# Kernel tuning notes

Hardware: AMD Instinct MI355X
Metric: run time of the kernel (lower is better)

## Reference

```python
import jax, jax.numpy as jnp
import numpy as np

DIM = 512; HEADS = 8; DH = 64; LAND = 256; PINV_ITERS = 6; RES_K = 33
NCLS = 4; FEAT = 1024; NPATCH = 16384

def layernorm(x, g, b, eps=1e-5):
    mu = x.mean(-1, keepdims=True)
    var = ((x - mu) ** 2).mean(-1, keepdims=True)
    return (x - mu) * jax.lax.rsqrt(var + eps) * g + b

def moore_penrose_pinv(x, iters):
    abs_x = jnp.abs(x)
    z = jnp.swapaxes(x, -1, -2) / (jnp.max(abs_x.sum(-1)) * jnp.max(abs_x.sum(-2)))
    I = jnp.eye(x.shape[-1], dtype=x.dtype)
    for _ in range(iters):
        xz = x @ z
        z = 0.25 * z @ (13 * I - xz @ (15 * I - xz @ (7 * I - xz)))
    return z

def nystrom_attention(x, qkv_w, out_w, out_b, res_w):
    b, n, _ = x.shape
    pad = (-n) % LAND  # left-pad to multiple of num_landmarks
    xp = jnp.pad(x, ((0, 0), (pad, 0), (0, 0)))
    N = n + pad
    q, k, v = jnp.split(xp @ qkv_w, 3, axis=-1)
    to_h = lambda t: t.reshape(b, N, HEADS, DH).transpose(0, 2, 1, 3)  # b h N d
    q = to_h(q) * (DH ** -0.5); k = to_h(k); v = to_h(v)
    l = N // LAND
    ql = q.reshape(b, HEADS, LAND, l, DH).mean(3)  # landmark means
    kl = k.reshape(b, HEADS, LAND, l, DH).mean(3)
    a1 = jax.nn.softmax(jnp.einsum('bhnd,bhmd->bhnm', q, kl), -1)
    a2 = jax.nn.softmax(jnp.einsum('bhld,bhmd->bhlm', ql, kl), -1)
    a3 = jax.nn.softmax(jnp.einsum('bhld,bhnd->bhln', ql, k), -1)
    out = (a1 @ moore_penrose_pinv(a2, PINV_ITERS)) @ (a3 @ v)  # b h N d
    res = jax.lax.conv_general_dilated(v, res_w, (1, 1), ((RES_K // 2, RES_K // 2), (0, 0)),
        dimension_numbers=('NCHW', 'OIHW', 'NCHW'), feature_group_count=HEADS)
    out = (out + res).transpose(0, 2, 1, 3).reshape(b, N, HEADS * DH)
    return (out @ out_w + out_b)[:, -n:]

def ppeg(x, w7, b7, w5, b5, w3, b3, Hh, Ww):
    B, _, C = x.shape
    cls, feat = x[:, :1], x[:, 1:]
    img = feat.transpose(0, 2, 1).reshape(B, C, Hh, Ww)
    def dw(w, bias, ksz):
        p = ksz // 2
        y = jax.lax.conv_general_dilated(img, w, (1, 1), ((p, p), (p, p)),
            dimension_numbers=('NCHW', 'OIHW', 'NCHW'), feature_group_count=C)
        return y + bias[None, :, None, None]
    y = img + dw(w7, b7, 7) + dw(w5, b5, 5) + dw(w3, b3, 3)
    return jnp.concatenate([cls, y.reshape(B, C, Hh * Ww).transpose(0, 2, 1)], 1)

def setup_inputs():
    ks = jax.random.split(jax.random.key(0), 16)
    p = lambda i, shape, s=0.02: jax.random.normal(ks[i], shape, jnp.float32) * s
    z = lambda shape: jnp.zeros(shape, jnp.float32)
    o = lambda shape: jnp.ones(shape, jnp.float32)
    return {
        'data_x': jax.random.normal(ks[0], (NPATCH, FEAT), jnp.float32),
        'fc1_w': p(1, (FEAT, DIM)), 'fc1_b': z((DIM,)),
        'cls_token': jax.random.normal(ks[2], (1, 1, DIM), jnp.float32),
        'l1_norm_g': o((DIM,)), 'l1_norm_b': z((DIM,)),
        'l1_qkv_w': p(3, (DIM, 3 * HEADS * DH)), 'l1_out_w': p(4, (HEADS * DH, DIM)), 'l1_out_b': z((DIM,)),
        'l1_res_w': p(5, (HEADS, 1, RES_K, 1)),
        'ppeg_w7': p(6, (DIM, 1, 7, 7)), 'ppeg_b7': z((DIM,)),
        'ppeg_w5': p(7, (DIM, 1, 5, 5)), 'ppeg_b5': z((DIM,)),
        'ppeg_w3': p(8, (DIM, 1, 3, 3)), 'ppeg_b3': z((DIM,)),
        'l2_norm_g': o((DIM,)), 'l2_norm_b': z((DIM,)),
        'l2_qkv_w': p(9, (DIM, 3 * HEADS * DH)), 'l2_out_w': p(10, (HEADS * DH, DIM)), 'l2_out_b': z((DIM,)),
        'l2_res_w': p(11, (HEADS, 1, RES_K, 1)),
        'norm_g': o((DIM,)), 'norm_b': z((DIM,)),
        'fc2_w': p(12, (DIM, NCLS)), 'fc2_b': z((NCLS,)),
    }

def reference(data_x, fc1_w, fc1_b, cls_token, l1_norm_g, l1_norm_b, l1_qkv_w, l1_out_w, l1_out_b, l1_res_w, ppeg_w7, ppeg_b7, ppeg_w5, ppeg_b5, ppeg_w3, ppeg_b3, l2_norm_g, l2_norm_b, l2_qkv_w, l2_out_w, l2_out_b, l2_res_w, norm_g, norm_b, fc2_w, fc2_b):
    h = jax.nn.relu(data_x[None] @ fc1_w + fc1_b)  # [1, N, 512]
    H = h.shape[1]
    _H = int(np.ceil(np.sqrt(H)))
    add = _H * _H - H
    h = jnp.concatenate([h, h[:, :add]], 1)  # square-pad by wrap
    cls = jnp.broadcast_to(cls_token, (h.shape[0], 1, DIM))
    h = jnp.concatenate([cls, h], 1)
    h = h + nystrom_attention(layernorm(h, l1_norm_g, l1_norm_b), l1_qkv_w, l1_out_w, l1_out_b, l1_res_w)
    h = ppeg(h, ppeg_w7, ppeg_b7, ppeg_w5, ppeg_b5, ppeg_w3, ppeg_b3, _H, _H)
    h = h + nystrom_attention(layernorm(h, l2_norm_g, l2_norm_b), l2_qkv_w, l2_out_w, l2_out_b, l2_res_w)
    h = layernorm(h, norm_g, norm_b)[:, 0]
    return h @ fc2_w + fc2_b
```

## Files before the change

### kernel.cpp

```cpp
#include <hip/hip_runtime.h>
#include <hip/hip_bf16.h>

#define NPAD 16640
#define TOK  16385
#define CDIM 512
#define NHEAD 8
#define DHEAD 64
#define NLAND 256
#define LFAC  65
#define PAD0  255
#define NCHUNK 65
#define CGRP 2
#define NCG 33

typedef __attribute__((ext_vector_type(8))) short sh8;
typedef __attribute__((ext_vector_type(4))) float f4;

__device__ __forceinline__ float wave_sum(float v){
  #pragma unroll
  for(int o=32;o;o>>=1) v += __shfl_xor(v,o);
  return v;
}
__device__ __forceinline__ float wave_max(float v){
  #pragma unroll
  for(int o=32;o;o>>=1) v = fmaxf(v, __shfl_xor(v,o));
  return v;
}

__device__ __forceinline__ unsigned bfbits(float x){
  unsigned u = __float_as_uint(x);
  return (u + 0x7fffu + ((u >> 16) & 1u)) >> 16;
}
__device__ __forceinline__ float bf2f(short s){
  return __uint_as_float(((unsigned)(unsigned short)s) << 16);
}
__device__ __forceinline__ sh8 pack8f(float4 a, float4 b){
  sh8 r;
  r[0]=(short)bfbits(a.x); r[1]=(short)bfbits(a.y); r[2]=(short)bfbits(a.z); r[3]=(short)bfbits(a.w);
  r[4]=(short)bfbits(b.x); r[5]=(short)bfbits(b.y); r[6]=(short)bfbits(b.z); r[7]=(short)bfbits(b.w);
  return r;
}
#define MFMA16(a,b,c) __builtin_amdgcn_mfma_f32_16x16x32_bf16(a,b,c,0,0,0)

__device__ __forceinline__ void gload16(const void* g, void* l){
  __builtin_amdgcn_global_load_lds(
      (const __attribute__((address_space(1))) void*)g,
      (__attribute__((address_space(3))) void*)l, 16, 0, 0);
}

#define BAR_LGKM() do{ \
  asm volatile("s_waitcnt lgkmcnt(0)" ::: "memory"); \
  __builtin_amdgcn_s_barrier(); \
  __builtin_amdgcn_sched_barrier(0); \
}while(0)

__global__ void k_copyrow(float* dst, const float* __restrict__ src){
  dst[threadIdx.x] = src[threadIdx.x];
}

__global__ __launch_bounds__(256) void k_f2b(const float* __restrict__ in,
    short* __restrict__ out, int n8){
  int i = blockIdx.x*256 + threadIdx.x;
  if(i < n8){
    float4 a = *(const float4*)(in + (size_t)i*8);
    float4 b = *(const float4*)(in + (size_t)i*8 + 4);
    *(sh8*)(out + (size_t)i*8) = pack8f(a, b);
  }
}

__global__ __launch_bounds__(256) void k_ln_pad(const float* __restrict__ A,
    const float* __restrict__ g, const float* __restrict__ b, short* __restrict__ B){
  int w = threadIdx.x >> 6, lane = threadIdx.x & 63;
  int row = blockIdx.x*4 + w;
  short* out = B + (size_t)row*CDIM;
  int c = lane*8;
  if(row < PAD0){
    sh8 z = {0,0,0,0,0,0,0,0};
    *(sh8*)(out + c) = z;
    return;
  }
  const float* x = A + (size_t)(row-PAD0)*CDIM;
  float4 v0 = *(const float4*)(x + c);
  float4 v1 = *(const float4*)(x + c + 4);
  float xs[8] = {v0.x,v0.y,v0.z,v0.w,v1.x,v1.y,v1.z,v1.w};
  float s = 0;
  #pragma unroll
  for(int i=0;i<8;i++) s += xs[i];
  s = wave_sum(s);
  float mu = s * (1.f/512.f);
  float vs = 0;
  #pragma unroll
  for(int i=0;i<8;i++){ float d = xs[i]-mu; vs += d*d; }
  vs = wave_sum(vs) * (1.f/512.f);
  float rs = rsqrtf(vs + 1e-5f);
  float4 g0 = *(const float4*)(g + c); float4 g1 = *(const float4*)(g + c + 4);
  float4 b0 = *(const float4*)(b + c); float4 b1 = *(const float4*)(b + c + 4);
  float gg[8] = {g0.x,g0.y,g0.z,g0.w,g1.x,g1.y,g1.z,g1.w};
  float bb[8] = {b0.x,b0.y,b0.z,b0.w,b1.x,b1.y,b1.z,b1.w};
  sh8 o;
  #pragma unroll
  for(int i=0;i<8;i++) o[i] = (short)bfbits((xs[i]-mu)*rs*gg[i] + bb[i]);
  *(sh8*)(out + c) = o;
}

template<int MODE>
__global__ __launch_bounds__(512) void k_gemm_g(const short* __restrict__ A, int lda,
    const short* __restrict__ WT, int K, const float* __restrict__ bias,
    void* out0v, void* out1v, void* out2v, int M){
  __shared__ short As[2][256*32];
  __shared__ short Bs[2][128*32];
  int t = threadIdx.x, lane = t & 63, wv = t >> 6, g = lane >> 4, l15 = lane & 15;
  int nwg = gridDim.x * gridDim.y;
  int orig = blockIdx.y * gridDim.x + blockIdx.x;
  int qc = nwg >> 3, rc = nwg & 7, xcd = orig & 7, loc = orig >> 3;
  int wgid = (xcd < rc ? xcd*(qc+1) : rc*(qc+1) + (xcd - rc)*qc) + loc;
  int row0 = (wgid / gridDim.x) * 256, n0 = (wgid % gridDim.x) * 128;
  int wm = (wv >> 1)*64, wn = (wv & 1)*64;
  int mq = lane >> 2, slot = lane & 3;

  auto stage = [&](int buf, int k0){
    #pragma unroll
    for(int c=0;c<2;c++){
      int m = c*128 + wv*16 + mq;
      int swz = (((m&3) ^ ((m>>2)&3)) << 4);
      int gr = row0 + m; if(gr >= M) gr = M-1;
      const char* srcA = (const char*)(A + (size_t)gr*lda + k0) + ((slot*16) ^ swz);
      gload16(srcA, (char*)As[buf] + (c*128 + wv*16)*64);
    }
    {
      int m = wv*16 + mq;
      int swz = (((m&3) ^ ((m>>2)&3)) << 4);
      const char* srcB = (const char*)(WT + (size_t)(n0+m)*K + k0) + ((slot*16) ^ swz);
      gload16(srcB, (char*)Bs[buf] + (wv*16)*64);
    }
  };

  f4 acc[4][4] = {};
  int nk = K >> 5;
  stage(0, 0);
  int cur = 0;
  for(int i=0; i<nk; i++){
    if(i+1 < nk){
      stage(cur^1, (i+1) << 5);
      asm volatile("s_waitcnt vmcnt(3)" ::: "memory");
    } else {
      asm volatile("s_waitcnt vmcnt(0)" ::: "memory");
    }
    __builtin_amdgcn_s_barrier();
    __builtin_amdgcn_sched_barrier(0);
    sh8 af[4], bf[4];
    #pragma unroll
    for(int mt=0; mt<4; mt++){
      int r = wm + mt*16 + l15;
      af[mt] = *(sh8*)((char*)As[cur] + r*64 + ((g*16) ^ (((r&3)^((r>>2)&3))<<4)));
    }
    #pragma unroll
    for(int nt=0; nt<4; nt++){
      int r = wn + nt*16 + l15;
      bf[nt] = *(sh8*)((char*)Bs[cur] + r*64 + ((g*16) ^ (((r&3)^((r>>2)&3))<<4)));
    }
    #pragma unroll
    for(int mt=0; mt<4; mt++)
      #pragma unroll
      for(int nt=0; nt<4; nt++)
        acc[mt][nt] = MFMA16(af[mt], bf[nt], acc[mt][nt]);
    BAR_LGKM();
    cur ^= 1;
  }
  #pragma unroll
  for(int mt=0; mt<4; mt++){
    #pragma unroll
    for(int r=0; r<4; r++){
      int gm = row0 + wm + mt*16 + g*4 + r;
      if(gm >= M) continue;
      #pragma unroll
      for(int nt=0; nt<4; nt++){
        int gn = n0 + wn + nt*16 + l15;
        float v = acc[mt][nt][r];
        if(MODE == 0){
          v += bias[gn];
          ((float*)out0v)[(size_t)gm*CDIM + gn] = v > 0.f ? v : 0.f;
        } else if(MODE == 1){
          int p = gn >> 9, rr = gn & 511;
          int hh = rr >> 6, dd = rr & 63;
          if(p == 0) v *= 0.125f;
          short* dst = (p==0) ? (short*)out0v : (p==1 ? (short*)out1v : (short*)out2v);
          dst[((size_t)hh*NPAD + gm)*DHEAD + dd] = (short)bfbits(v);
        } else {
          ((float*)out0v)[(size_t)gm*CDIM + gn] += v + bias[gn];
        }
      }
    }
  }
}

__global__ void k_landmark2(const short* __restrict__ Qb, const short* __restrict__ Kb,
    float* __restrict__ ql, float* __restrict__ kl){
  int bidx = blockIdx.x;
  int sel = bidx >> 11;
  int loc = bidx & 2047;
  int h = loc >> 8, m = loc & 255, d = threadIdx.x;
  const short* src = (sel ? Kb : Qb) + ((size_t)h*NPAD + (size_t)m*LFAC)*DHEAD + d;
  float s = 0;
  for(int j=0;j<LFAC;j++) s += bf2f(src[(size_t)j*DHEAD]);
  (sel ? kl : ql)[(size_t)loc*DHEAD + d] = s * (1.f/LFAC);
}

__global__ __launch_bounds__(256) void k_a2_mfma(const float* __restrict__ ql,
    const float* __restrict__ kl, float* __restrict__ a2, short* __restrict__ a2bf){
  __shared__ short klL[256*64];
  int q = blockIdx.x, h = blockIdx.y;
  int t = threadIdx.x, lane = t & 63, wv = t >> 6, g = lane >> 4, l15 = lane & 15;
  const float* qlh = ql + (size_t)h*NLAND*DHEAD;
  const float* klh = kl + (size_t)h*NLAND*DHEAD;
  #pragma unroll
  for(int i=0;i<8;i++){
    int gi = t + i*256;
    int n = gi >> 3, db = (gi & 7)*8;
    float4 a = *(const float4*)(klh + (size_t)n*DHEAD + db);
    float4 b = *(const float4*)(klh + (size_t)n*DHEAD + db + 4);
    *(sh8*)((char*)klL + n*128 + ((db*2) ^ ((n&7)<<4))) = pack8f(a, b);
  }
  __syncthreads();
  int row0 = q*64 + wv*16;
  sh8 aQ[2];
  #pragma unroll
  for(int kk=0; kk<2; kk++){
    const float* p = qlh + (size_t)(row0 + l15)*DHEAD + kk*32 + g*8;
    aQ[kk] = pack8f(*(const float4*)p, *(const float4*)(p+4));
  }
  f4 acc[16];
  #pragma unroll
  for(int nt=0; nt<16; nt++){
    f4 s = {};
    #pragma unroll
    for(int kk=0; kk<2; kk++){
      int n = nt*16 + l15;
      sh8 b = *(sh8*)((char*)klL + n*128 + ((kk*64 + g*16) ^ ((n&7)<<4)));
      s = MFMA16(aQ[kk], b, s);
    }
    acc[nt] = s;
  }
  float den[4] = {0,0,0,0};
  #pragma unroll
  for(int nt=0; nt<16; nt++)
    #pragma unroll
    for(int r=0; r<4; r++){
      float e = __expf(acc[nt][r]);
      acc[nt][r] = e;
      den[r] += e;
    }
  #pragma unroll
  for(int r=0; r<4; r++){
    float d_ = den[r];
    d_ += __shfl_xor(d_,1); d_ += __shfl_xor(d_,2);
    d_ += __shfl_xor(d_,4); d_ += __shfl_xor(d_,8);
    den[r] = 1.f/d_;
  }
  #pragma unroll
  for(int nt=0; nt<16; nt++)
    #pragma unroll
    for(int r=0; r<4; r++){
      int row = row0 + g*4 + r;
      int col = nt*16 + l15;
      float v = acc[nt][r]*den[r];
      size_t idx = ((size_t)h*NLAND + row)*NLAND + col;
      a2[idx] = v;
      a2bf[idx] = (short)bfbits(v);
    }
}

__global__ void k_colmax(const float* __restrict__ a2, float* __restrict__ hmax){
  __shared__ float red[4];
  int h = blockIdx.x, t = threadIdx.x;
  const float* p = a2 + (size_t)h*65536 + t;
  float s = 0;
  for(int m=0;m<256;m++) s += p[(size_t)m*256];
  float mx = wave_max(s);
  if((t & 63) == 0) red[t>>6] = mx;
  __syncthreads();
  if(t == 0) hmax[h] = fmaxf(fmaxf(red[0],red[1]), fmaxf(red[2],red[3]));
}
__global__ void k_zinit(const float* __restrict__ a2, const float* __restrict__ hmax,
                        short* __restrict__ z){
  int h = blockIdx.y;
  int idx = blockIdx.x*256 + threadIdx.x;
  int m = idx >> 8, j = idx & 255;
  float mx = hmax[0];
  #pragma unroll
  for(int i=1;i<8;i++) mx = fmaxf(mx, hmax[i]);
  z[(size_t)h*65536 + idx] = (short)bfbits(a2[(size_t)h*65536 + (size_t)j*256 + m] / mx);
}

template<int TRANS, int F32OUT>
__global__ __launch_bounds__(256) void k_pgemm(const short* __restrict__ A,
    const short* __restrict__ B, short* __restrict__ C, float* __restrict__ Cf,
    float alpha, float beta){
  __shared__ short As[64*32];
  __shared__ short Bs[64*32];
  int bh = blockIdx.z;
  const short* Ah = A + (size_t)bh*65536;
  const short* Bh = B + (size_t)bh*65536;
  int m0 = blockIdx.y*64, n0 = blockIdx.x*64;
  int t = threadIdx.x, lane = t & 63, wv = t >> 6, g = lane >> 4, l15 = lane & 15;
  f4 acc[4] = {};
  for(int k0=0; k0<256; k0+=32){
    {
      int m = t >> 2, kb = (t & 3)*8;
      sh8 av = *(const sh8*)(Ah + (size_t)(m0+m)*256 + k0 + kb);
      int swz = (((m&3)^((m>>2)&3))<<4);
      *(sh8*)((char*)As + m*64 + ((kb*2)^swz)) = av;
    }
    {
      int kr = t >> 3, nb = (t & 7)*8;
      sh8 bv = *(const sh8*)(Bh + (size_t)(k0+kr)*256 + n0 + nb);
      #pragma unroll
      for(int e=0;e<8;e++){
        int n = nb + e;
        short sv = bv[e];
        if(TRANS){
          float f = ((k0+kr == n0+n) ? alpha : 0.f) - bf2f(sv);
          sv = (short)bfbits(f);
        }
        int swz = (((n&3)^((n>>2)&3))<<4);
        *(short*)((char*)Bs + n*64 + ((kr*2)^swz)) = sv;
      }
    }
    __syncthreads();
    int rm = wv*16 + l15;
    sh8 af = *(sh8*)((char*)As + rm*64 + ((g*16) ^ (((rm&3)^((rm>>2)&3))<<4)));
    #pragma unroll
    for(int nt=0; nt<4; nt++){
      int n = nt*16 + l15;
      sh8 bf = *(sh8*)((char*)Bs + n*64 + ((g*16) ^ (((n&3)^((n>>2)&3))<<4)));
      acc[nt] = MFMA16(af, bf, acc[nt]);
    }
    __syncthreads();
  }
  size_t hoff = (size_t)bh*65536;
  #pragma unroll
  for(int nt=0; nt<4; nt++)
    #pragma unroll
    for(int r=0; r<4; r++){
      size_t idx = hoff + (size_t)(m0 + wv*16 + g*4 + r)*256 + n0 + nt*16 + l15;
      float v = acc[nt][r]*beta;
      if(F32OUT) Cf[idx] = v;
      else       C[idx] = (short)bfbits(v);
    }
}

template<int TRANS, int OUTT>
__global__ __launch_bounds__(256) void k_sgemm2(const float* __restrict__ A,
    const float* __restrict__ B, float* __restrict__ C,
    int M, int N, int K, long sA, long sB, long sC, float alpha, float beta){
  __shared__ float As[32][68];
  __shared__ float Bs[32][68];
  int bh = blockIdx.z;
  const float* Ah = A + (size_t)bh*sA;
  const float* Bh = B + (size_t)bh*sB;
  float* Ch = C + (size_t)bh*sC;
  int m0 = blockIdx.y*64, n0 = blockIdx.x*64;
  int t = threadIdx.x, tx = t & 15, ty = t >> 4;
  float acc[4][4] = {};
  for(int k0=0; k0<K; k0+=32){
    #pragma unroll
    for(int u=0; u<2; u++){
      int idx = t + u*256;
      int r = idx >> 3, cb = (idx & 7) * 4;
      float4 va = *(const float4*)(Ah + (size_t)(m0+r)*K + k0 + cb);
      As[cb+0][r]=va.x; As[cb+1][r]=va.y; As[cb+2][r]=va.z; As[cb+3][r]=va.w;
      int kr = idx >> 4, nb = (idx & 15) * 4;
      float4 w = *(const float4*)(Bh + (size_t)(k0+kr)*N + n0 + nb);
      if(TRANS){
        int gk = k0 + kr;
        w.x = ((gk==n0+nb+0)?alpha:0.f) - w.x;
        w.y = ((gk==n0+nb+1)?alpha:0.f) - w.y;
        w.z = ((gk==n0+nb+2)?alpha:0.f) - w.z;
        w.w = ((gk==n0+nb+3)?alpha:0.f) - w.w;
      }
      *(float4*)&Bs[kr][nb] = w;
    }
    __syncthreads();
    #pragma unroll
    for(int k=0;k<32;k++){
      float a[4], b[4];
      *(float4*)a = *(const float4*)&As[k][ty*4];
      *(float4*)b = *(const float4*)&Bs[k][tx*4];
      #pragma unroll
      for(int i=0;i<4;i++)
        #pragma unroll
        for(int j=0;j<4;j++) acc[i][j] += a[i]*b[j];
    }
    __syncthreads();
  }
  #pragma unroll
  for(int i=0;i<4;i++){
    #pragma unroll
    for(int j=0;j<4;j++){
      int gm = m0 + ty*4 + i, gn = n0 + tx*4 + j;
      float v = acc[i][j] * beta;
      if(OUTT) Ch[(size_t)gn*M + gm] = v;
      else     Ch[(size_t)gm*N + gn] = v;
    }
  }
}

__global__ __launch_bounds__(256) void k_a1_mfma(const short* __restrict__ Qb,
    const float* __restrict__ kl, const float* __restrict__ w2t, short* __restrict__ F){
  __shared__ short klL[128*64];
  __shared__ short w2L[64*128];
  __shared__ short pL[4][16*128];
  int h = blockIdx.y, n0 = blockIdx.x*128;
  int t = threadIdx.x, lane = t & 63, wv = t >> 6, g = lane >> 4, l15 = lane & 15;
  const float* klh = kl + (size_t)h*NLAND*DHEAD;
  const float* w2h = w2t + (size_t)h*DHEAD*NLAND;
  const short* qbase = Qb + (size_t)h*NPAD*DHEAD;
  sh8 aQ[2][2];
  #pragma unroll
  for(int st=0; st<2; st++)
    #pragma unroll
    for(int kk=0; kk<2; kk++)
      aQ[st][kk] = *(const sh8*)(qbase +
          (size_t)(n0 + wv*32 + st*16 + l15)*DHEAD + kk*32 + g*8);
  f4 accO[2][4] = {};
  float den[2][4] = {};
  short* pw = pL[wv];
  for(int half=0; half<2; half++){
    __syncthreads();
    #pragma unroll
    for(int it=0; it<4; it++){
      int gi = t + it*256;
      int m = gi >> 3, db = (gi & 7) * 8;
      const float* p = klh + (size_t)(half*128 + m)*DHEAD + db;
      *(sh8*)((char*)klL + m*128 + ((db*2) ^ ((m&7)<<4))) =
          pack8f(*(const float4*)p, *(const float4*)(p+4));
      int d = gi >> 4, mb = (gi & 15) * 8;
      const float* p2 = w2h + (size_t)d*NLAND + half*128 + mb;
      *(sh8*)((char*)w2L + d*256 + ((mb*2) ^ ((d&7)<<4))) =
          pack8f(*(const float4*)p2, *(const float4*)(p2+4));
    }
    __syncthreads();
    #pragma unroll
    for(int st=0; st<2; st++){
      #pragma unroll
      for(int mt=0; mt<8; mt++){
        f4 s = {};
        #pragma unroll
        for(int kk=0; kk<2; kk++){
          int m = mt*16 + l15;
          sh8 b = *(sh8*)((char*)klL + m*128 + ((kk*64 + g*16) ^ ((m&7)<<4)));
          s = MFMA16(aQ[st][kk], b, s);
        }
        #pragma unroll
        for(int r=0; r<4; r++){
          float e = __expf(s[r]);
          den[st][r] += e;
          int n = g*4 + r;
          *(short*)((char*)pw + n*256 + (((mt*16+l15)*2) ^ ((n&7)<<4))) = (short)bfbits(e);
        }
      }
      #pragma unroll
      for(int ks=0; ks<4; ks++){
        sh8 aP = *(sh8*)((char*)pw + l15*256 + ((ks*64 + g*16) ^ ((l15&7)<<4)));
        #pragma unroll
        for(int dt=0; dt<4; dt++){
          int d = dt*16 + l15;
          sh8 bW = *(sh8*)((char*)w2L + d*256 + ((ks*64 + g*16) ^ ((d&7)<<4)));
          accO[st][dt] = MFMA16(aP, bW, accO[st][dt]);
        }
      }
    }
  }
  #pragma unroll
  for(int st=0; st<2; st++)
    #pragma unroll
    for(int r=0; r<4; r++){
      float d_ = den[st][r];
      d_ += __shfl_xor(d_,1); d_ += __shfl_xor(d_,2);
      d_ += __shfl_xor(d_,4); d_ += __shfl_xor(d_,8);
      den[st][r] = 1.f/d_;
    }
  #pragma unroll
  for(int st=0; st<2; st++)
    #pragma unroll
    for(int dt=0; dt<4; dt++)
      #pragma unroll
      for(int r=0; r<4; r++){
        int row = n0 + wv*32 + st*16 + g*4 + r;
        F[(size_t)row*CDIM + h*DHEAD + dt*16 + l15] =
            (short)bfbits(accO[st][dt][r]*den[st][r]);
      }
}

__global__ __launch_bounds__(512) void k_a3v_mfma(const float* __restrict__ ql,
    const short* __restrict__ Kb, const short* __restrict__ Vb,
    float* __restrict__ numP, float* __restrict__ denP){
  __shared__ short kL[128*64];
  __shared__ short vL[64*128];
  __shared__ short pL[8][16*128];
  int h = blockIdx.x, cg = blockIdx.y;
  int t = threadIdx.x, lane = t & 63, wv = t >> 6, g = lane >> 4, l15 = lane & 15;
  int r0 = (wv & 3)*64 + (wv >> 2)*32;
  const float* qlh = ql + (size_t)h*NLAND*DHEAD;
  sh8 aQ[2][2];
  #pragma unroll
  for(int st=0; st<2; st++)
    #pragma unroll
    for(int kk=0; kk<2; kk++){
      const float* p = qlh + (size_t)(r0 + st*16 + l15)*DHEAD + kk*32 + g*8;
      aQ[st][kk] = pack8f(*(const float4*)p, *(const float4*)(p+4));
    }
  f4 accO[2][4] = {};
  float den[2][4] = {};
  short* pw = pL[wv];

  int km[2], kdb[2];
  #pragma unroll
  for(int it=0; it<2; it++){
    int gi = t + it*512;
    km[it] = gi >> 3; kdb[it] = (gi & 7) * 8;
  }
  int vmp = (t & 63)*2, vdg = (t >> 6)*8;

  sh8 kreg[2], vreg[2];
  auto ldregs = [&](int ph){
    int c = cg*CGRP + (ph >> 1), half = ph & 1;
    const short* Kh = Kb + ((size_t)h*NPAD + (size_t)c*256 + half*128)*DHEAD;
    const short* Vh = Vb + ((size_t)h*NPAD + (size_t)c*256 + half*128)*DHEAD;
    #pragma unroll
    for(int it=0; it<2; it++)
      kreg[it] = *(const sh8*)(Kh + (size_t)km[it]*DHEAD + kdb[it]);
    vreg[0] = *(const sh8*)(Vh + (size_t)vmp*DHEAD + vdg);
    vreg[1] = *(const sh8*)(Vh + (size_t)(vmp+1)*DHEAD + vdg);
  };

  int nph = 2*CGRP;
  if(cg*CGRP + ((nph-1) >> 1) >= NCHUNK) nph = 2;
  ldregs(0);
  for(int ph=0; ph<nph; ph++){
    BAR_LGKM();
    #pragma unroll
    for(int it=0; it<2; it++)
      *(sh8*)((char*)kL + km[it]*128 + ((kdb[it]*2) ^ ((km[it]&7)<<4))) = kreg[it];
    {
      sh8 v0 = vreg[0], v1 = vreg[1];
      #pragma unroll
      for(int i=0;i<8;i++){
        int d = vdg + i;
        unsigned pk = ((unsigned)(unsigned short)v0[i]) |
                      (((unsigned)(unsigned short)v1[i]) << 16);
        *(unsigned*)((char*)vL + d*256 + ((vmp*2) ^ ((d&7)<<4))) = pk;
      }
    }
    if(ph+1 < nph) ldregs(ph+1);
    BAR_LGKM();
    #pragma unroll
    for(int st=0; st<2; st++){
      #pragma unroll
      for(int mt=0; mt<8; mt++){
        f4 s = {};
        #pragma unroll
        for(int kk=0; kk<2; kk++){
          int m = mt*16 + l15;
          sh8 b = *(sh8*)((char*)kL + m*128 + ((kk*64 + g*16) ^ ((m&7)<<4)));
          s = MFMA16(aQ[st][kk], b, s);
        }
        #pragma unroll
        for(int r=0; r<4; r++){
          float e = __expf(s[r]);
          den[st][r] += e;
          int n = g*4 + r;
          *(short*)((char*)pw + n*256 + (((mt*16+l15)*2) ^ ((n&7)<<4))) = (short)bfbits(e);
        }
      }
      #pragma unroll
      for(int ks=0; ks<4; ks++){
        sh8 aP = *(sh8*)((char*)pw + l15*256 + ((ks*64 + g*16) ^ ((l15&7)<<4)));
        #pragma unroll
        for(int dt=0; dt<4; dt++){
          int d = dt*16 + l15;
          sh8 bV = *(sh8*)((char*)vL + d*256 + ((ks*64 + g*16) ^ ((d&7)<<4)));
          accO[st][dt] = MFMA16(aP, bV, accO[st][dt]);
        }
      }
    }
  }
  #pragma unroll
  for(int st=0; st<2; st++)
    #pragma unroll
    for(int r=0; r<4; r++){
      float d_ = den[st][r];
      d_ += __shfl_xor(d_,1); d_ += __shfl_xor(d_,2);
      d_ += __shfl_xor(d_,4); d_ += __shfl_xor(d_,8);
      den[st][r] = d_;
    }
  size_t base = ((size_t)h*NCG + cg)*NLAND;
  #pragma unroll
  for(int st=0; st<2; st++){
    #pragma unroll
    for(int r=0; r<4; r++){
      int row = r0 + st*16 + g*4 + r;
      if(l15 == 0) denP[base + row] = den[st][r];
      #pragma unroll
      for(int dt=0; dt<4; dt++)
        numP[(base + row)*DHEAD + dt*16 + l15] = accO[st][dt][r];
    }
  }
}

__global__ void k_a3v_comb(const float* __restrict__ numP, const float* __restrict__ denP,
                           float* __restrict__ a3v){
  int bidx = blockIdx.x;
  int h = bidx >> 8, m = bidx & 255;
  int d = threadIdx.x;
  float s = 0.f, den = 0.f;
  for(int c=0;c<NCG;c++){
    s += numP[(((size_t)h*NCG + c)*NLAND + m)*DHEAD + d];
    den += denP[((size_t)h*NCG + c)*NLAND + m];
  }
  a3v[((size_t)h*NLAND + m)*DHEAD + d] = s / den;
}

__global__ __launch_bounds__(256) void k_resconv(const short* __restrict__ Vb,
    const float* __restrict__ rw, short* __restrict__ F){
  __shared__ float vs[96][64];
  int n0 = blockIdx.x*64, h = blockIdx.y;
  int t = threadIdx.x;
  const short* vh = Vb + (size_t)h*NPAD*DHEAD;
  #pragma unroll
  for(int i=0;i<3;i++){
    int idx = t + i*256;
    int r = idx >> 3, dg = (idx & 7)*8;
    int n = n0 - 16 + r;
    sh8 v = {0,0,0,0,0,0,0,0};
    if(n>=0 && n<NPAD) v = *(const sh8*)(vh + (size_t)n*DHEAD + dg);
    #pragma unroll
    for(int e=0;e<8;e++) vs[r][dg+e] = bf2f(v[e]);
  }
  float w[33];
  #pragma unroll
  for(int j=0;j<33;j++) w[j] = rw[h*33+j];
  __syncthreads();
  int d = t & 63, grp = t >> 6;
  float f0[16];
  #pragma unroll
  for(int rr=0;rr<16;rr++){
    int n = n0 + grp*16 + rr;
    f0[rr] = bf2f(F[(size_t)n*CDIM + h*DHEAD + d]);
  }
  float in[48];
  #pragma unroll
  for(int x=0;x<48;x++) in[x] = vs[grp*16 + x][d];
  #pragma unroll
  for(int rr=0;rr<16;rr++){
    float acc = 0.f;
    #pragma unroll
    for(int j=0;j<33;j++) acc += w[j]*in[rr+j];
    int n = n0 + grp*16 + rr;
    F[(size_t)n*CDIM + h*DHEAD + d] = (short)bfbits(f0[rr] + acc);
  }
}

__global__ void k_transb5(
    const float* s0, short* d0, int R0, int C0,
    const float* s1, short* d1, int R1, int C1,
    const float* s2, short* d2, int R2, int C2,
    const float* s3, short* d3, int R3, int C3,
    const float* s4, short* d4, int R4, int C4){
  const float* in; short* out; int R, C;
  switch(blockIdx.z){
    case 0: in=s0; out=d0; R=R0; C=C0; break;
    case 1: in=s1; out=d1; R=R1; C=C1; break;
    case 2: in=s2; out=d2; R=R2; C=C2; break;
    case 3: in=s3; out=d3; R=R3; C=C3; break;
    default: in=s4; out=d4; R=R4; C=C4; break;
  }
  __shared__ float tile[32][33];
  int r0 = blockIdx.x*32, c0 = blockIdx.y*32;
  if(r0 >= R || c0 >= C) return;
  int tx = threadIdx.x, ty = threadIdx.y;
  #pragma unroll
  for(int r=0;r<4;r++) tile[ty + r*8][tx] = in[(size_t)(r0 + ty + r*8)*C + c0 + tx];
  __syncthreads();
  #pragma unroll
  for(int r=0;r<4;r++)
    out[(size_t)(c0 + ty + r*8)*R + r0 + tx] = (short)bfbits(tile[tx][ty + r*8]);
}

__global__ __launch_bounds__(256) void k_ppeg2(const float* __restrict__ X,
    const float* __restrict__ w7, const float* __restrict__ b7,
    const float* __restrict__ w5, const float* __restrict__ b5,
    const float* __restrict__ w3, const float* __restrict__ b3,
    float* __restrict__ Y){
  __shared__ float patch[484][20];
  int cg = blockIdx.y;
  int ti = blockIdx.x >> 3, tj = blockIdx.x & 7;
  int t = threadIdx.x;
  int i0 = ti*16 - 3, j0 = tj*16 - 3;
  for(int idx = t; idx < 1936; idx += 256){
    int p = idx >> 2, cq = (idx & 3) * 4;
    int gi = i0 + p/22, gj = j0 + p%22;
    float4 v = make_float4(0.f,0.f,0.f,0.f);
    if(gi>=0 && gi<128 && gj>=0 && gj<128)
      v = *(const float4*)(X + (size_t)(gi*128+gj)*CDIM + cg*16 + cq);
    *(float4*)&patch[p][cq] = v;
  }
  int c = t & 15, sg = t >> 4;
  int cglob = cg*16 + c;
  float wr[83];
  #pragma unroll
  for(int k=0;k<49;k++) wr[k] = w7[cglob*49+k];
  #pragma unroll
  for(int k=0;k<25;k++) wr[49+k] = w5[cglob*25+k];
  #pragma unroll
  for(int k=0;k<9;k++)  wr[74+k] = w3[cglob*9+k];
  float bsum = b7[cglob] + b5[cglob] + b3[cglob];
  __syncthreads();
  float acc[16];
  #pragma unroll
  for(int j=0;j<16;j++) acc[j] = patch[(sg+3)*22 + (j+3)][c] + bsum;
  #pragma unroll
  for(int a=0;a<7;a++)
    #pragma unroll
    for(int x=0;x<22;x++){
      float vv = patch[(sg+a)*22 + x][c];
      #pragma unroll
      for(int bq=0;bq<7;bq++){
        int j = x - bq;
        if(j>=0 && j<16) acc[j] += wr[a*7+bq]*vv;
      }
    }
  #pragma unroll
  for(int a=0;a<5;a++)
    #pragma unroll
    for(int x=1;x<21;x++){
      float vv = patch[(sg+a+1)*22 + x][c];
      #pragma unroll
      for(int bq=0;bq<5;bq++){
        int j = x - 1 - bq;
        if(j>=0 && j<16) acc[j] += wr[49+a*5+bq]*vv;
      }
    }
  #pragma unroll
  for(int a=0;a<3;a++)
    #pragma unroll
    for(int x=2;x<20;x++){
      float vv = patch[(sg+a+2)*22 + x][c];
      #pragma unroll
      for(int bq=0;bq<3;bq++){
        int j = x - 2 - bq;
        if(j>=0 && j<16) acc[j] += wr[74+a*3+bq]*vv;
      }
    }
  #pragma unroll
  for(int j=0;j<16;j++)
    Y[(size_t)((ti*16+sg)*128 + tj*16+j)*CDIM + cglob] = acc[j];
}

__global__ __launch_bounds__(512) void k_final(const float* __restrict__ A,
    const float* __restrict__ g, const float* __restrict__ b,
    const float* __restrict__ w, const float* __restrict__ bias,
    float* __restrict__ outp){
  __shared__ float red[8];
  int t = threadIdx.x, wv = t >> 6;
  float x = A[t];
  float s = wave_sum(x);
  if((t & 63) == 0) red[wv] = s;
  __syncthreads();
  float mu = 0;
  #pragma unroll
  for(int i=0;i<8;i++) mu += red[i];
  mu *= (1.f/512.f);
  __syncthreads();
  float dx = x - mu;
  s = wave_sum(dx*dx);
  if((t & 63) == 0) red[wv] = s;
  __syncthreads();
  float var = 0;
  #pragma unroll
  for(int i=0;i<8;i++) var += red[i];
  var *= (1.f/512.f);
  float xn = dx * rsqrtf(var + 1e-5f) * g[t] + b[t];
  __syncthreads();
  for(int o=0;o<4;o++){
    s = wave_sum(xn * w[t*4 + o]);
    if((t & 63) == 0) red[wv] = s;
    __syncthreads();
    if(t == 0){
      float r = 0;
      #pragma unroll
      for(int i=0;i<8;i++) r += red[i];
      outp[o] = r + bias[o];
    }
    __syncthreads();
  }
}

extern "C" void kernel_launch(void* const* d_in, const int* in_sizes, int n_in,
                              void* d_out, int out_size, void* d_ws, size_t ws_size,
                              hipStream_t stream) {
  (void)in_sizes; (void)n_in; (void)out_size; (void)ws_size;
  const float* data_x = (const float*)d_in[0];
  const float* fc1_w  = (const float*)d_in[1];
  const float* fc1_b  = (const float*)d_in[2];
  const float* cls_tk = (const float*)d_in[3];
  const float* ng[2]  = {(const float*)d_in[4],  (const float*)d_in[16]};
  const float* nb[2]  = {(const float*)d_in[5],  (const float*)d_in[17]};
  const float* qkvw[2]= {(const float*)d_in[6],  (const float*)d_in[18]};
  const float* outw[2]= {(const float*)d_in[7],  (const float*)d_in[19]};
  const float* outb[2]= {(const float*)d_in[8],  (const float*)d_in[20]};
  const float* resw[2]= {(const float*)d_in[9],  (const float*)d_in[21]};
  const float* w7 = (const float*)d_in[10]; const float* pb7 = (const float*)d_in[11];
  const float* w5 = (const float*)d_in[12]; const float* pb5 = (const float*)d_in[13];
  const float* w3 = (const float*)d_in[14]; const float* pb3 = (const float*)d_in[15];
  const float* norm_g = (const float*)d_in[22];
  const float* norm_b = (const float*)d_in[23];
  const float* fc2_w  = (const float*)d_in[24];
  const float* fc2_b  = (const float*)d_in[25];

  float* ws = (float*)d_ws;
  float* Ab   = ws;
  float* Bb   = Ab + (size_t)TOK*CDIM;
  float* Fb   = Bb + (size_t)TOK*CDIM;
  short* Fbf  = (short*)(Fb + (size_t)NPAD*CDIM);
  short* lnX  = Fbf + (size_t)NPAD*CDIM;
  short* Qb   = lnX + (size_t)NPAD*CDIM;
  short* Kb   = Qb  + (size_t)NPAD*CDIM;
  short* Vb   = Kb  + (size_t)NPAD*CDIM;
  short* dxb  = Vb  + (size_t)NPAD*CDIM;
  float* qlb  = (float*)(dxb + (size_t)16384*1024);
  float* klb  = qlb + NHEAD*NLAND*DHEAD;
  float* a2b  = klb + NHEAD*NLAND*DHEAD;
  float* z0b  = a2b + NHEAD*NLAND*NLAND;
  float* z1b  = z0b + NHEAD*NLAND*NLAND;
  float* Xb_  = z1b + NHEAD*NLAND*NLAND;
  float* Tb_  = Xb_ + NHEAD*NLAND*NLAND;
  float* Ub_  = Tb_ + NHEAD*NLAND*NLAND;
  float* a3vb = Ub_ + NHEAD*NLAND*NLAND;
  float* w2tb = a3vb + NHEAD*NLAND*DHEAD;
  float* denP = w2tb + NHEAD*DHEAD*NLAND;
  float* hmax = denP + NHEAD*NCG*NLAND;
  float* scal = hmax + 8;
  short* fc1T = (short*)(scal + 8);
  short* qkvT0= fc1T + 512*1024;
  short* qkvT1= qkvT0 + 1536*512;
  short* outT0= qkvT1 + 1536*512;
  short* outT1= outT0 + 512*512;
  short* qkvT[2] = {qkvT0, qkvT1};
  short* outT[2] = {outT0, outT1};

  const int HB = NHEAD*NLAND*NLAND;
  short* zb0  = (short*)z0b;  short* zb1  = zb0 + HB;
  short* xb   = (short*)z1b;  short* tb   = xb + HB;
  short* ub   = (short*)Xb_;  short* a2bf = ub + HB;
  float* zf   = Tb_;

  k_transb5<<<dim3(32,48,5), dim3(32,8), 0, stream>>>(
      fc1_w, fc1T, 1024, 512,
      qkvw[0], qkvT0, 512, 1536,
      qkvw[1], qkvT1, 512, 1536,
      outw[0], outT0, 512, 512,
      outw[1], outT1, 512, 512);
  k_f2b<<<8192, 256, 0, stream>>>(data_x, dxb, 16384*1024/8);

  k_copyrow<<<1, 512, 0, stream>>>(Ab, cls_tk);
  k_gemm_g<0><<<dim3(4, 64), 512, 0, stream>>>(dxb, 1024, fc1T, 1024, fc1_b,
                                               Ab + CDIM, nullptr, nullptr, 16384);
  float* base[2]  = {Ab, Bb};
  for(int L=0; L<2; L++){
    k_ln_pad<<<NPAD/4, 256, 0, stream>>>(base[L], ng[L], nb[L], lnX);
    k_gemm_g<1><<<dim3(12, 65), 512, 0, stream>>>(lnX, CDIM, qkvT[L], CDIM, nullptr,
                                                  Qb, Kb, Vb, NPAD);
    k_landmark2<<<2*NHEAD*NLAND, 64, 0, stream>>>(Qb, Kb, qlb, klb);
    k_a2_mfma<<<dim3(4, NHEAD), 256, 0, stream>>>(qlb, klb, a2b, a2bf);
    k_colmax<<<NHEAD, 256, 0, stream>>>(a2b, hmax);
    k_zinit<<<dim3(256, NHEAD), 256, 0, stream>>>(a2b, hmax, zb0);
    short* zc = zb0; short* zn = zb1;
    for(int it=0; it<6; it++){
      k_pgemm<0,0><<<dim3(4,4,NHEAD), 256, 0, stream>>>(a2bf, zc, xb, nullptr, 0.f, 1.f);
      k_pgemm<1,0><<<dim3(4,4,NHEAD), 256, 0, stream>>>(xb, xb, tb, nullptr, 7.f, 1.f);
      k_pgemm<1,0><<<dim3(4,4,NHEAD), 256, 0, stream>>>(xb, tb, ub, nullptr, 15.f, 1.f);
      if(it < 5){
        k_pgemm<1,0><<<dim3(4,4,NHEAD), 256, 0, stream>>>(zc, ub, zn, nullptr, 13.f, 0.25f);
        short* tmp = zc; zc = zn; zn = tmp;
      } else {
        k_pgemm<1,1><<<dim3(4,4,NHEAD), 256, 0, stream>>>(zc, ub, nullptr, zf, 13.f, 0.25f);
      }
    }
    k_a3v_mfma<<<dim3(NHEAD, NCG), 512, 0, stream>>>(qlb, Kb, Vb, Fb, denP);
    k_a3v_comb<<<NHEAD*NLAND, 64, 0, stream>>>(Fb, denP, a3vb);
    k_sgemm2<0,1><<<dim3(1,4,NHEAD), 256, 0, stream>>>(zf, a3vb, w2tb, 256,64,256,
                                                       65536,16384,16384, 0.f, 1.f);
    k_a1_mfma<<<dim3(130, NHEAD), 256, 0, stream>>>(Qb, klb, w2tb, Fbf);
    k_resconv<<<dim3(260, NHEAD), 256, 0, stream>>>(Vb, resw[L], Fbf);
    k_gemm_g<2><<<dim3(4, 65), 512, 0, stream>>>(Fbf + (size_t)PAD0*CDIM, CDIM,
                                                 outT[L], CDIM, outb[L],
                                                 base[L], nullptr, nullptr, TOK);
    if(L == 0){
      k_ppeg2<<<dim3(64, 32), 256, 0, stream>>>(Ab + CDIM, w7, pb7, w5, pb5, w3, pb3,
                                                Bb + CDIM);
      k_copyrow<<<1, 512, 0, stream>>>(Bb, Ab);
    }
  }
  k_final<<<1, 512, 0, stream>>>(Bb, norm_g, norm_b, fc2_w, fc2_b, (float*)d_out);
}
```

Before: 915.3 us.

## Fuse pinv iteration GEMMs into one persistent kernel with grid barriers

Replaces the 24 separate small pinv GEMM launches per layer with a single persistent kernel of 128 blocks that synchronises between GEMM stages using atomic-counter grid barriers. Phase counters are zeroed once at start and reused across the two layers through a generation target. This is meant to remove kernel launch overhead and tail gaps between tiny dependent GEMMs. It relies on all 128 blocks being co-resident, since the spin barrier would deadlock otherwise, and it turns the compile-time template flags into runtime branches.

```diff
diff --git a/kernel.cpp b/kernel.cpp
--- a/kernel.cpp
+++ b/kernel.cpp
@@ -54,9 +54,21 @@
   __builtin_amdgcn_sched_barrier(0); \
 }while(0)
 
+__device__ __forceinline__ void gridbar(unsigned* c, unsigned tgt){
+  __syncthreads();
+  if(threadIdx.x == 0){
+    __threadfence();
+    atomicAdd(c, 1u);
+    while(atomicAdd(c, 0u) < tgt){ __builtin_amdgcn_s_sleep(2); }
+    __threadfence();
+  }
+  __syncthreads();
+}
+
 __global__ void k_copyrow(float* dst, const float* __restrict__ src){
   dst[threadIdx.x] = src[threadIdx.x];
 }
+__global__ void k_zero32(unsigned* c){ c[threadIdx.x] = 0u; }
 
 __global__ __launch_bounds__(256) void k_f2b(const float* __restrict__ in,
     short* __restrict__ out, int n8){
@@ -292,16 +304,10 @@
   z[(size_t)h*65536 + idx] = (short)bfbits(a2[(size_t)h*65536 + (size_t)j*256 + m] / mx);
 }
 
-template<int TRANS, int F32OUT>
-__global__ __launch_bounds__(256) void k_pgemm(const short* __restrict__ A,
-    const short* __restrict__ B, short* __restrict__ C, float* __restrict__ Cf,
-    float alpha, float beta){
-  __shared__ short As[64*32];
-  __shared__ short Bs[64*32];
-  int bh = blockIdx.z;
-  const short* Ah = A + (size_t)bh*65536;
-  const short* Bh = B + (size_t)bh*65536;
-  int m0 = blockIdx.y*64, n0 = blockIdx.x*64;
+__device__ __forceinline__ void pinv_tile(const short* __restrict__ Ah,
+    const short* __restrict__ Bh, short* __restrict__ Ch, float* __restrict__ Cf,
+    int m0, int n0, float alpha, float beta, int trans, int f32out,
+    short* As, short* Bs){
   int t = threadIdx.x, lane = t & 63, wv = t >> 6, g = lane >> 4, l15 = lane & 15;
   f4 acc[4] = {};
   for(int k0=0; k0<256; k0+=32){
@@ -318,7 +324,7 @@
       for(int e=0;e<8;e++){
         int n = nb + e;
         short sv = bv[e];
-        if(TRANS){
+        if(trans){
           float f = ((k0+kr == n0+n) ? alpha : 0.f) - bf2f(sv);
           sv = (short)bfbits(f);
         }
@@ -337,16 +343,44 @@
     }
     __syncthreads();
   }
-  size_t hoff = (size_t)bh*65536;
   #pragma unroll
   for(int nt=0; nt<4; nt++)
     #pragma unroll
     for(int r=0; r<4; r++){
-      size_t idx = hoff + (size_t)(m0 + wv*16 + g*4 + r)*256 + n0 + nt*16 + l15;
+      size_t idx = (size_t)(m0 + wv*16 + g*4 + r)*256 + n0 + nt*16 + l15;
       float v = acc[nt][r]*beta;
-      if(F32OUT) Cf[idx] = v;
-      else       C[idx] = (short)bfbits(v);
-    }
+      if(f32out) Cf[idx] = v;
+      else       Ch[idx] = (short)bfbits(v);
+    }
+}
+
+__global__ __launch_bounds__(256) void k_pinv(const short* __restrict__ a2bf,
+    short* z0, short* z1, short* xb, short* tb, short* ub, float* zf,
+    unsigned* cnt, unsigned gen){
+  __shared__ short As[64*32];
+  __shared__ short Bs[64*32];
+  int bh = blockIdx.z;
+  size_t off = (size_t)bh*65536;
+  int m0 = blockIdx.y*64, n0 = blockIdx.x*64;
+  const short* a2h = a2bf + off;
+  short* zc = z0; short* zn = z1;
+  int ph = 0;
+  unsigned tgt = gen*128u;
+  for(int it=0; it<6; it++){
+    pinv_tile(a2h, zc+off, xb+off, nullptr, m0, n0, 0.f, 1.f, 0, 0, As, Bs);
+    gridbar(cnt+ph, tgt); ph++;
+    pinv_tile(xb+off, xb+off, tb+off, nullptr, m0, n0, 7.f, 1.f, 1, 0, As, Bs);
+    gridbar(cnt+ph, tgt); ph++;
+    pinv_tile(xb+off, tb+off, ub+off, nullptr, m0, n0, 15.f, 1.f, 1, 0, As, Bs);
+    gridbar(cnt+ph, tgt); ph++;
+    if(it < 5){
+      pinv_tile(zc+off, ub+off, zn+off, nullptr, m0, n0, 13.f, 0.25f, 1, 0, As, Bs);
+      gridbar(cnt+ph, tgt); ph++;
+      short* tmp = zc; zc = zn; zn = tmp;
+    } else {
+      pinv_tile(zc+off, ub+off, nullptr, zf+off, m0, n0, 13.f, 0.25f, 1, 1, As, Bs);
+    }
+  }
 }
 
 template<int TRANS, int OUTT>
@@ -841,7 +875,8 @@
   float* denP = w2tb + NHEAD*DHEAD*NLAND;
   float* hmax = denP + NHEAD*NCG*NLAND;
   float* scal = hmax + 8;
-  short* fc1T = (short*)(scal + 8);
+  unsigned* cntw = (unsigned*)(scal + 8);
+  short* fc1T = (short*)(cntw + 32);
   short* qkvT0= fc1T + 512*1024;
   short* qkvT1= qkvT0 + 1536*512;
   short* outT0= qkvT1 + 1536*512;
@@ -855,6 +890,7 @@
   short* ub   = (short*)Xb_;  short* a2bf = ub + HB;
   float* zf   = Tb_;
 
+  k_zero32<<<1, 32, 0, stream>>>(cntw);
   k_transb5<<<dim3(32,48,5), dim3(32,8), 0, stream>>>(
       fc1_w, fc1T, 1024, 512,
       qkvw[0], qkvT0, 512, 1536,
@@ -875,18 +911,8 @@
     k_a2_mfma<<<dim3(4, NHEAD), 256, 0, stream>>>(qlb, klb, a2b, a2bf);
     k_colmax<<<NHEAD, 256, 0, stream>>>(a2b, hmax);
     k_zinit<<<dim3(256, NHEAD), 256, 0, stream>>>(a2b, hmax, zb0);
-    short* zc = zb0; short* zn = zb1;
-    for(int it=0; it<6; it++){
-      k_pgemm<0,0><<<dim3(4,4,NHEAD), 256, 0, stream>>>(a2bf, zc, xb, nullptr, 0.f, 1.f);
-      k_pgemm<1,0><<<dim3(4,4,NHEAD), 256, 0, stream>>>(xb, xb, tb, nullptr, 7.f, 1.f);
-      k_pgemm<1,0><<<dim3(4,4,NHEAD), 256, 0, stream>>>(xb, tb, ub, nullptr, 15.f, 1.f);
-      if(it < 5){
-        k_pgemm<1,0><<<dim3(4,4,NHEAD), 256, 0, stream>>>(zc, ub, zn, nullptr, 13.f, 0.25f);
-        short* tmp = zc; zc = zn; zn = tmp;
-      } else {
-        k_pgemm<1,1><<<dim3(4,4,NHEAD), 256, 0, stream>>>(zc, ub, nullptr, zf, 13.f, 0.25f);
-      }
-    }
+    k_pinv<<<dim3(4,4,NHEAD), 256, 0, stream>>>(a2bf, zb0, zb1, xb, tb, ub, zf,
+                                                cntw, (unsigned)(L+1));
     k_a3v_mfma<<<dim3(NHEAD, NCG), 512, 0, stream>>>(qlb, Kb, Vb, Fb, denP);
     k_a3v_comb<<<NHEAD*NLAND, 64, 0, stream>>>(Fb, denP, a3vb);
     k_sgemm2<0,1><<<dim3(1,4,NHEAD), 256, 0, stream>>>(zf, a3vb, w2tb, 256,64,256,
```

Result: slower. 1.327 ms (+45.0%).
